# Performance work log

Hardware: AMD Instinct MI355X
Metric: run time of the kernel (lower is better)

## Reference

```python
import jax, jax.numpy as jnp
import numpy as np
from functools import partial

D_MODEL = 1024
D_HIDDEN = 4096
N_BLOCKS = 4
D_VOCAB = 32000
BATCH = 2
SEQ = 2048
LN_EPS = 1e-5
LRELU_SLOPE = 0.01  # torch nn.LeakyReLU default


def setup_inputs() -> dict:
    key = jax.random.key(0)
    ks = jax.random.split(key, 16)
    d, h, L, v = D_MODEL, D_HIDDEN, N_BLOCKS, D_VOCAB
    scale = d ** 0.5
    inp = {
        "tokens": jax.random.randint(ks[0], (BATCH, SEQ), 0, v, dtype=jnp.int64)
                  if jax.config.jax_enable_x64 else
                  jax.random.randint(ks[0], (BATCH, SEQ), 0, v, dtype=jnp.int32),
        "emb": jax.random.normal(ks[1], (v, d), jnp.float32) * 0.02,
        # per-block stacked params (leading axis = layer) for lax.scan
        "qk": jax.random.normal(ks[2], (L, d, d), jnp.float32) / scale,
        "ov": jax.random.normal(ks[3], (L, d, d), jnp.float32) / scale,
        "w_up": jax.random.normal(ks[4], (L, d, h), jnp.float32) / scale,
        "b_up": jnp.zeros((L, h), jnp.float32),
        "w_hid": jax.random.normal(ks[5], (L, h, h), jnp.float32) / (h ** 0.5),
        "b_hid": jnp.zeros((L, h), jnp.float32),
        "w_down": jax.random.normal(ks[6], (L, h, d), jnp.float32) / (h ** 0.5),
        "b_down": jnp.zeros((L, d), jnp.float32),
        "ln1_g": jnp.ones((L, d), jnp.float32),
        "ln1_b": jnp.zeros((L, d), jnp.float32),
        "ln2_g": jnp.ones((L, d), jnp.float32),
        "ln2_b": jnp.zeros((L, d), jnp.float32),
    }
    return inp


def _layer_norm(x, g, b):
    mu = jnp.mean(x, axis=-1, keepdims=True)
    var = jnp.mean(jnp.square(x - mu), axis=-1, keepdims=True)
    return (x - mu) * jax.lax.rsqrt(var + LN_EPS) * g + b


def _forward(tokens, emb, qk, ov, w_up, b_up, w_hid, b_hid, w_down, b_down,
             ln1_g, ln1_b, ln2_g, ln2_b):
    x = emb[tokens]                                   # [B, S, D]
    seq = tokens.shape[1]
    scale = jnp.asarray(D_MODEL ** 0.5, x.dtype)
    causal = jnp.tril(jnp.ones((seq, seq), bool))     # True = keep

    def block(x, p):
        (qk, ov, w_up, b_up, w_hid, b_hid, w_down, b_down,
         g1, b1, g2, b2) = p
        h = _layer_norm(x, g1, b1)
        # attention: (h @ qk @ h^T) / sqrt(d), causal mask, softmax, @ h @ ov
        scores = jnp.einsum('bsd,de,bte->bst', h, qk, h) / scale
        scores = jnp.where(causal, scores, -jnp.inf)
        attn = jax.nn.softmax(scores, axis=-1)
        x = x + jnp.einsum('bst,btd,de->bse', attn, h, ov)
        # MLP with LeakyReLU after every layer (incl. output)
        m = _layer_norm(x, g2, b2)
        m = jax.nn.leaky_relu(m @ w_up + b_up, LRELU_SLOPE)
        m = jax.nn.leaky_relu(m @ w_hid + b_hid, LRELU_SLOPE)
        m = jax.nn.leaky_relu(m @ w_down + b_down, LRELU_SLOPE)
        return x + m, None

    params = (qk, ov, w_up, b_up, w_hid, b_hid, w_down, b_down,
              ln1_g, ln1_b, ln2_g, ln2_b)
    x, _ = jax.lax.scan(block, x, params)
    return x @ emb.T                                  # [B, S, V] logits


@jax.jit
def reference(tokens, emb, qk, ov, w_up, b_up, w_hid, b_hid, w_down, b_down,
              ln1_g, ln1_b, ln2_g, ln2_b):
    return _forward(tokens, emb, qk, ov, w_up, b_up, w_hid, b_hid,
                    w_down, b_down, ln1_g, ln1_b, ln2_g, ln2_b)
```

## Files before the change

### kernel.cpp

```cpp
#include <hip/hip_runtime.h>

#define BS   4096
#define SEQL 2048
#define DM   1024
#define DH   4096
#define NV   32000

using u16 = unsigned short;

typedef __attribute__((ext_vector_type(8))) short bf16x8;
typedef __attribute__((ext_vector_type(4))) float f32x4;

__device__ __forceinline__ u16 f2b(float f) {
  union { float f; unsigned u; } c; c.f = f;
  unsigned u = c.u;
  u = (u + 0x7FFFu + ((u >> 16) & 1u)) >> 16;
  return (u16)u;
}

__device__ __forceinline__ void gld16(const u16* g, u16* l) {
  __builtin_amdgcn_global_load_lds(
      (__attribute__((address_space(1))) void*)(void*)const_cast<u16*>(g),
      (__attribute__((address_space(3))) void*)l, 16, 0, 0);
}

__global__ __launch_bounds__(256) void k_embed(const int* __restrict__ tok,
                                               const float* __restrict__ emb,
                                               float* __restrict__ x) {
  const long row = blockIdx.x;
  const long e = tok[row];
  ((float4*)(x + row * DM))[threadIdx.x] = ((const float4*)(emb + e * DM))[threadIdx.x];
}

__global__ __launch_bounds__(256) void k_cvt(const float* __restrict__ in,
                                             u16* __restrict__ out, int n4) {
  int i = blockIdx.x * 256 + threadIdx.x;
  if (i < n4) {
    float4 v = ((const float4*)in)[i];
    ushort4 o;
    o.x = f2b(v.x); o.y = f2b(v.y); o.z = f2b(v.z); o.w = f2b(v.w);
    ((ushort4*)out)[i] = o;
  }
}

__global__ __launch_bounds__(256) void k_ln(const float* __restrict__ x,
                                            const float* __restrict__ g,
                                            const float* __restrict__ b,
                                            u16* __restrict__ out) {
  const long row = blockIdx.x;
  const int t = threadIdx.x;
  float4 v = ((const float4*)(x + row * DM))[t];
  float s  = v.x + v.y + v.z + v.w;
  float q2 = v.x*v.x + v.y*v.y + v.z*v.z + v.w*v.w;
#pragma unroll
  for (int o = 1; o < 64; o <<= 1) { s += __shfl_xor(s, o); q2 += __shfl_xor(q2, o); }
  __shared__ float rs_[4], rq_[4];
  const int lane = t & 63, wid = t >> 6;
  if (lane == 0) { rs_[wid] = s; rq_[wid] = q2; }
  __syncthreads();
  s  = rs_[0] + rs_[1] + rs_[2] + rs_[3];
  q2 = rq_[0] + rq_[1] + rq_[2] + rq_[3];
  const float mu   = s * (1.f / 1024.f);
  const float var  = q2 * (1.f / 1024.f) - mu * mu;
  const float rstd = rsqrtf(var + 1e-5f);
  float4 gg = ((const float4*)g)[t];
  float4 bb = ((const float4*)b)[t];
  ushort4 o;
  o.x = f2b((v.x - mu) * rstd * gg.x + bb.x);
  o.y = f2b((v.y - mu) * rstd * gg.y + bb.y);
  o.z = f2b((v.z - mu) * rstd * gg.z + bb.z);
  o.w = f2b((v.w - mu) * rstd * gg.w + bb.w);
  ((ushort4*)(out + row * DM))[t] = o;
}

__device__ __forceinline__ u16 to_b16(float v) { return f2b(v); }
__device__ __forceinline__ u16 to_b16(u16 v)   { return v; }

template <typename T>
__global__ __launch_bounds__(256) void k_transpose(const T* __restrict__ in,
                                                   u16* __restrict__ out,
                                                   int R, int C, long inz, long outz) {
  __shared__ u16 tile[32][33];
  const T* ip = in + (long)blockIdx.z * inz;
  u16* op = out + (long)blockIdx.z * outz;
  const int tx = threadIdx.x & 31, ty = threadIdx.x >> 5;
  const long c0 = (long)blockIdx.x * 32, r0 = (long)blockIdx.y * 32;
#pragma unroll
  for (int i = 0; i < 4; ++i)
    tile[ty + i * 8][tx] = to_b16(ip[(r0 + ty + i * 8) * C + c0 + tx]);
  __syncthreads();
#pragma unroll
  for (int i = 0; i < 4; ++i)
    op[(c0 + ty + i * 8) * R + r0 + tx] = tile[tx][ty + i * 8];
}

__global__ __launch_bounds__(256) void k_softmax(const float* __restrict__ sc,
                                                 u16* __restrict__ at) {
  const int r = blockIdx.x;
  const long z = blockIdx.y;
  const int t = threadIdx.x;
  const float* row = sc + (z * SEQL + r) * SEQL;
  u16* orow = at + (z * SEQL + r) * SEQL;
  float vals[8];
  float mx = -3.4e38f;
#pragma unroll
  for (int i = 0; i < 8; ++i) {
    int c = i * 256 + t;
    float v = (c <= r) ? row[c] : -3.4e38f;
    vals[i] = v;
    mx = fmaxf(mx, v);
  }
#pragma unroll
  for (int o = 1; o < 64; o <<= 1) mx = fmaxf(mx, __shfl_xor(mx, o));
  __shared__ float rm[4], rsum[4];
  const int lane = t & 63, wid = t >> 6;
  if (lane == 0) rm[wid] = mx;
  __syncthreads();
  mx = fmaxf(fmaxf(rm[0], rm[1]), fmaxf(rm[2], rm[3]));
  float sum = 0.f;
#pragma unroll
  for (int i = 0; i < 8; ++i) {
    int c = i * 256 + t;
    float e = (c <= r) ? __expf(vals[i] - mx) : 0.f;
    vals[i] = e;
    sum += e;
  }
#pragma unroll
  for (int o = 1; o < 64; o <<= 1) sum += __shfl_xor(sum, o);
  if (lane == 0) rsum[wid] = sum;
  __syncthreads();
  sum = rsum[0] + rsum[1] + rsum[2] + rsum[3];
  const float inv = 1.f / sum;
#pragma unroll
  for (int i = 0; i < 8; ++i) orow[i * 256 + t] = f2b(vals[i] * inv);
}

template <int EPI, bool BIAS, bool LRELU, int CAUSAL>
__global__ __launch_bounds__(256, 2) void k_gemm_bt(
    const u16* __restrict__ A, const u16* __restrict__ B, void* __restrict__ C,
    const float* __restrict__ bias, int K, int N,
    long sAz, long sBz, long sCz, float scale) {
  __shared__ u16 lA[128 * 32];
  __shared__ u16 lB[128 * 32];
  const int t = threadIdx.x;
  const long z = blockIdx.z;
  const long row0 = (long)blockIdx.x * 128;
  const long col0 = (long)blockIdx.y * 128;
  if (CAUSAL == 1 && col0 > row0 + 127) return;
  const int Klim = (CAUSAL == 2) ? min(K, (int)row0 + 128) : K;
  const u16* Ab = A + z * sAz;
  const u16* Bb = B + z * sBz;

  const int rr = t >> 2;
  const int c8 = (t & 3) * 8;
  const u16* gA0 = Ab + (row0 + rr) * K + c8;
  const u16* gA1 = Ab + (row0 + 64 + rr) * K + c8;
  const u16* gB0 = Bb + (col0 + rr) * K + c8;
  const u16* gB1 = Bb + (col0 + 64 + rr) * K + c8;
  u16* sA0 = &lA[rr * 32 + c8];
  u16* sA1 = &lA[(64 + rr) * 32 + c8];
  u16* sB0 = &lB[rr * 32 + c8];
  u16* sB1 = &lB[(64 + rr) * 32 + c8];

  const int lane = t & 63;
  const int w = t >> 6;
  const int wr = (w >> 1) * 64, wc = (w & 1) * 64;
  const int fr = lane & 15;
  const int fk = (lane >> 4) * 8;

  f32x4 acc[4][4] = {};

  for (int k0 = 0; k0 < Klim; k0 += 32) {
    gld16(gA0 + k0, sA0);
    gld16(gA1 + k0, sA1);
    gld16(gB0 + k0, sB0);
    gld16(gB1 + k0, sB1);
    __syncthreads();
    bf16x8 av[4], bv[4];
#pragma unroll
    for (int m = 0; m < 4; ++m) av[m] = *(const bf16x8*)&lA[(wr + m * 16 + fr) * 32 + fk];
#pragma unroll
    for (int n = 0; n < 4; ++n) bv[n] = *(const bf16x8*)&lB[(wc + n * 16 + fr) * 32 + fk];
#pragma unroll
    for (int m = 0; m < 4; ++m)
#pragma unroll
      for (int n = 0; n < 4; ++n)
        acc[m][n] = __builtin_amdgcn_mfma_f32_16x16x32_bf16(av[m], bv[n], acc[m][n], 0, 0, 0);
    __syncthreads();
  }

  const int er = (lane >> 4) * 4;
  const int ec = lane & 15;
#pragma unroll
  for (int m = 0; m < 4; ++m) {
#pragma unroll
    for (int n = 0; n < 4; ++n) {
#pragma unroll
      for (int j = 0; j < 4; ++j) {
        long r = row0 + wr + m * 16 + er + j;
        long c = col0 + wc + n * 16 + ec;
        float v = acc[m][n][j] * scale;
        if (BIAS)  v += bias[c];
        if (LRELU) v = v > 0.f ? v : 0.01f * v;
        if (EPI == 0)      ((float*)C)[z * sCz + r * (long)N + c] = v;
        else if (EPI == 1) ((u16*)C)[z * sCz + r * (long)N + c] = f2b(v);
        else               ((float*)C)[z * sCz + r * (long)N + c] += v;
      }
    }
  }
}

template <int EPI, bool BIAS, bool LRELU>
__global__ __launch_bounds__(512, 2) void k_gemm256(
    const u16* __restrict__ A, const u16* __restrict__ B, void* __restrict__ C,
    const float* __restrict__ bias, int K, int N, float scale) {
  __shared__ u16 S[2][2][16384];
  const int t = threadIdx.x;
  const int lane = t & 63;
  const int w = t >> 6;
  const int wr = w >> 2;
  const int wc = w & 3;
  const long row0 = (long)blockIdx.x * 256;
  const long col0 = (long)blockIdx.y * 256;
  const int nt = K >> 6;

  const u16* pA[4];
  const u16* pB[4];
  int ldsoff[4];
#pragma unroll
  for (int i = 0; i < 4; ++i) {
    int d = t * 16 + i * 8192;
    int dx = d ^ (((d >> 7) & 7) << 4);
    int srow = dx >> 7;
    int scol = (dx & 127) >> 1;
    ldsoff[i] = d >> 1;
    pA[i] = A + (row0 + srow) * (long)K + scol;
    pB[i] = B + (col0 + srow) * (long)K + scol;
  }

  const int fr = lane & 15;
  const int fky = lane >> 4;
  const int axor = (fr & 7) << 4;
  const int abase = (wr * 128 + fr) * 128 + fky * 16;
  const int bbase = (wc * 64 + fr) * 128 + fky * 16;

  f32x4 acc[8][4] = {};

  auto STAGE = [&](int b) {
    u16* SA = &S[b][0][0];
    u16* SB = &S[b][1][0];
#pragma unroll
    for (int i = 0; i < 4; ++i) gld16(pA[i], SA + ldsoff[i]);
#pragma unroll
    for (int i = 0; i < 4; ++i) gld16(pB[i], SB + ldsoff[i]);
#pragma unroll
    for (int i = 0; i < 4; ++i) { pA[i] += 64; pB[i] += 64; }
  };

  auto COMPUTE = [&](int b) {
    const char* Ab = (const char*)&S[b][0][0];
    const char* Bb = (const char*)&S[b][1][0];
    bf16x8 bv[8];
#pragma unroll
    for (int n = 0; n < 4; ++n)
#pragma unroll
      for (int kk = 0; kk < 2; ++kk)
        bv[n * 2 + kk] = *(const bf16x8*)(Bb + ((bbase + n * 2048 + kk * 64) ^ axor));
    __builtin_amdgcn_s_setprio(1);
#pragma unroll
    for (int m = 0; m < 8; ++m) {
      bf16x8 a0 = *(const bf16x8*)(Ab + ((abase + m * 2048) ^ axor));
      bf16x8 a1 = *(const bf16x8*)(Ab + ((abase + m * 2048 + 64) ^ axor));
#pragma unroll
      for (int n = 0; n < 4; ++n)
        acc[m][n] = __builtin_amdgcn_mfma_f32_16x16x32_bf16(a0, bv[n * 2], acc[m][n], 0, 0, 0);
#pragma unroll
      for (int n = 0; n < 4; ++n)
        acc[m][n] = __builtin_amdgcn_mfma_f32_16x16x32_bf16(a1, bv[n * 2 + 1], acc[m][n], 0, 0, 0);
    }
    __builtin_amdgcn_s_setprio(0);
  };

  STAGE(0);
  __syncthreads();
  int cur = 0;
  for (int tt = 0; tt < nt; ++tt) {
    if (tt + 1 < nt) STAGE(cur ^ 1);
    COMPUTE(cur);
    __syncthreads();
    cur ^= 1;
  }

  const int er = (lane >> 4) * 4;
  const int ec = lane & 15;
#pragma unroll
  for (int m = 0; m < 8; ++m) {
#pragma unroll
    for (int n = 0; n < 4; ++n) {
#pragma unroll
      for (int j = 0; j < 4; ++j) {
        long r = row0 + wr * 128 + m * 16 + er + j;
        long c = col0 + wc * 64 + n * 16 + ec;
        float v = acc[m][n][j] * scale;
        if (BIAS)  v += bias[c];
        if (LRELU) v = v > 0.f ? v : 0.01f * v;
        if (EPI == 0)      ((float*)C)[r * (long)N + c] = v;
        else if (EPI == 1) ((u16*)C)[r * (long)N + c] = f2b(v);
        else               ((float*)C)[r * (long)N + c] += v;
      }
    }
  }
}

extern "C" void kernel_launch(void* const* d_in, const int* in_sizes, int n_in,
                              void* d_out, int out_size, void* d_ws, size_t ws_size,
                              hipStream_t stream) {
  const int*   tokens = (const int*)d_in[0];
  const float* emb    = (const float*)d_in[1];
  const float* qk     = (const float*)d_in[2];
  const float* ov     = (const float*)d_in[3];
  const float* wup    = (const float*)d_in[4];
  const float* bup    = (const float*)d_in[5];
  const float* whid   = (const float*)d_in[6];
  const float* bhid   = (const float*)d_in[7];
  const float* wdown  = (const float*)d_in[8];
  const float* bdown  = (const float*)d_in[9];
  const float* g1     = (const float*)d_in[10];
  const float* b1     = (const float*)d_in[11];
  const float* g2     = (const float*)d_in[12];
  const float* b2     = (const float*)d_in[13];

  char* Ob = (char*)d_out;
  float* scores = (float*)(Ob + 0);
  u16*   attn   = (u16*)(Ob + 33554432);
  u16*   m1     = (u16*)(Ob + 50331648);
  u16*   m2     = (u16*)(Ob + 83886080);
  u16*   qkT    = (u16*)(Ob + 117440512);
  u16*   ovT    = (u16*)(Ob + 125829120);
  u16*   upT    = (u16*)(Ob + 134217728);
  u16*   hidT   = (u16*)(Ob + 167772160);
  u16*   downT  = (u16*)(Ob + 301989888);
  float* xres   = (float*)(Ob + 335544320);
  u16*   h      = (u16*)(Ob + 352321536);
  u16*   hT     = (u16*)(Ob + 360710144);
  u16*   q      = (u16*)(Ob + 369098752);
  u16*   attnV  = (u16*)(Ob + 377487360);

  u16* embB = (u16*)d_ws;
  u16* xB   = (u16*)((char*)d_ws + 65536000);

  k_embed<<<dim3(BS), 256, 0, stream>>>(tokens, emb, xres);
  k_cvt<<<dim3(32000), 256, 0, stream>>>(emb, embB, 8192000);

  k_transpose<float><<<dim3(32, 32, 4),   256, 0, stream>>>(qk,    qkT,   1024, 1024, 1048576,  1048576);
  k_transpose<float><<<dim3(32, 32, 4),   256, 0, stream>>>(ov,    ovT,   1024, 1024, 1048576,  1048576);
  k_transpose<float><<<dim3(128, 32, 4),  256, 0, stream>>>(wup,   upT,   1024, 4096, 4194304,  4194304);
  k_transpose<float><<<dim3(128, 128, 4), 256, 0, stream>>>(whid,  hidT,  4096, 4096, 16777216, 16777216);
  k_transpose<float><<<dim3(32, 128, 4),  256, 0, stream>>>(wdown, downT, 4096, 1024, 4194304,  4194304);

  for (int l = 0; l < 4; ++l) {
    k_ln<<<dim3(BS), 256, 0, stream>>>(xres, g1 + l * 1024, b1 + l * 1024, h);
    k_transpose<u16><<<dim3(32, 64, 2), 256, 0, stream>>>(h, hT, 2048, 1024, 2048L * 1024, 1024L * 2048);
    k_gemm_bt<1, false, false, 0><<<dim3(32, 8, 1), 256, 0, stream>>>(
        h, qkT + (long)l * 1048576, q, nullptr, 1024, 1024, 0, 0, 0, 0.03125f);
    k_gemm_bt<0, false, false, 1><<<dim3(16, 16, 2), 256, 0, stream>>>(
        q, h, scores, nullptr, 1024, 2048, 2048L * 1024, 2048L * 1024, 2048L * 2048, 1.f);
    k_softmax<<<dim3(2048, 2), 256, 0, stream>>>(scores, attn);
    k_gemm_bt<1, false, false, 2><<<dim3(16, 8, 2), 256, 0, stream>>>(
        attn, hT, attnV, nullptr, 2048, 1024, 2048L * 2048, 1024L * 2048, 2048L * 1024, 1.f);
    k_gemm_bt<2, false, false, 0><<<dim3(32, 8, 1), 256, 0, stream>>>(
        attnV, ovT + (long)l * 1048576, xres, nullptr, 1024, 1024, 0, 0, 0, 1.f);

    k_ln<<<dim3(BS), 256, 0, stream>>>(xres, g2 + l * 1024, b2 + l * 1024, h);
    k_gemm256<1, true, true><<<dim3(16, 16), 512, 0, stream>>>(
        h, upT + (long)l * 4194304, m1, bup + l * 4096, 1024, 4096, 1.f);
    k_gemm256<1, true, true><<<dim3(16, 16), 512, 0, stream>>>(
        m1, hidT + (long)l * 16777216, m2, bhid + l * 4096, 4096, 4096, 1.f);
    k_gemm_bt<2, true, true, 0><<<dim3(32, 8, 1), 256, 0, stream>>>(
        m2, downT + (long)l * 4194304, xres, bdown + l * 1024, 4096, 1024, 0, 0, 0, 1.f);
  }

  k_cvt<<<dim3(4096), 256, 0, stream>>>(xres, xB, 1048576);
  k_gemm256<0, false, false><<<dim3(16, 125), 512, 0, stream>>>(
      xB, embB, (float*)d_out, nullptr, 1024, 32000, 1.f);
}
```

Baseline: 2.120 ms.

## Restructure 256x256 GEMM into four-phase pipelined schedule with split-K LDS halves

Rewrites the main loop of the 256-tile GEMM so each K-step of 64 is split into two 32-wide halves and two M-halves, giving four phases. Each phase issues LDS reads, then one quarter of the next tile's global-to-LDS loads, then 16 MFMAs, with explicit s_barrier and vmcnt waits in place of __syncthreads. The LDS layout moves to 64-byte rows with a smaller XOR swizzle, offsets are precomputed, and launch bounds drop to one block per CU. The aim is finer interleaving of memory loads with MFMA work, at the cost of fewer resident waves and the risk of races if the vmcnt counting is wrong.

```diff
diff --git a/kernel.cpp b/kernel.cpp
--- a/kernel.cpp
+++ b/kernel.cpp
@@ -211,10 +211,11 @@
 }
 
 template <int EPI, bool BIAS, bool LRELU>
-__global__ __launch_bounds__(512, 2) void k_gemm256(
+__global__ __launch_bounds__(512, 1) void k_gemm256(
     const u16* __restrict__ A, const u16* __restrict__ B, void* __restrict__ C,
     const float* __restrict__ bias, int K, int N, float scale) {
-  __shared__ u16 S[2][2][16384];
+  __shared__ u16 S[65536];
+  char* Sc = (char*)&S[0];
   const int t = threadIdx.x;
   const int lane = t & 63;
   const int w = t >> 6;
@@ -224,72 +225,94 @@
   const long col0 = (long)blockIdx.y * 256;
   const int nt = K >> 6;
 
-  const u16* pA[4];
-  const u16* pB[4];
-  int ldsoff[4];
-#pragma unroll
-  for (int i = 0; i < 4; ++i) {
+  int srow[2], scol[2], ldsb[2];
+#pragma unroll
+  for (int i = 0; i < 2; ++i) {
     int d = t * 16 + i * 8192;
-    int dx = d ^ (((d >> 7) & 7) << 4);
-    int srow = dx >> 7;
-    int scol = (dx & 127) >> 1;
-    ldsoff[i] = d >> 1;
-    pA[i] = A + (row0 + srow) * (long)K + scol;
-    pB[i] = B + (col0 + srow) * (long)K + scol;
-  }
+    int dx = d ^ (((d >> 7) & 3) << 4);
+    srow[i] = dx >> 6;
+    scol[i] = (dx & 63) >> 1;
+    ldsb[i] = d;
+  }
+  const u16* Abase = A + row0 * (long)K;
+  const u16* Bbase = B + col0 * (long)K;
+
+  auto stage = [&](int opb, int kh, int buf, int kb) {
+#pragma unroll
+    for (int i = 0; i < 2; ++i) {
+      const u16* src = (opb ? Bbase : Abase) + (long)srow[i] * K + kb + kh * 32 + scol[i];
+      u16* dst = &S[(buf * 4 + opb * 2 + kh) * 8192 + (ldsb[i] >> 1)];
+      gld16(src, dst);
+    }
+  };
 
   const int fr = lane & 15;
   const int fky = lane >> 4;
-  const int axor = (fr & 7) << 4;
-  const int abase = (wr * 128 + fr) * 128 + fky * 16;
-  const int bbase = (wc * 64 + fr) * 128 + fky * 16;
+  const int axor = ((fr >> 1) & 3) << 4;
+  int aoff[8], boff[4];
+#pragma unroll
+  for (int m = 0; m < 8; ++m)
+    aoff[m] = (((wr * 128 + m * 16 + fr) * 64) + fky * 16) ^ axor;
+#pragma unroll
+  for (int n = 0; n < 4; ++n)
+    boff[n] = (((wc * 64 + n * 16 + fr) * 64) + fky * 16) ^ axor;
 
   f32x4 acc[8][4] = {};
 
-  auto STAGE = [&](int b) {
-    u16* SA = &S[b][0][0];
-    u16* SB = &S[b][1][0];
-#pragma unroll
-    for (int i = 0; i < 4; ++i) gld16(pA[i], SA + ldsoff[i]);
-#pragma unroll
-    for (int i = 0; i < 4; ++i) gld16(pB[i], SB + ldsoff[i]);
-#pragma unroll
-    for (int i = 0; i < 4; ++i) { pA[i] += 64; pB[i] += 64; }
-  };
-
-  auto COMPUTE = [&](int b) {
-    const char* Ab = (const char*)&S[b][0][0];
-    const char* Bb = (const char*)&S[b][1][0];
-    bf16x8 bv[8];
-#pragma unroll
-    for (int n = 0; n < 4; ++n)
-#pragma unroll
-      for (int kk = 0; kk < 2; ++kk)
-        bv[n * 2 + kk] = *(const bf16x8*)(Bb + ((bbase + n * 2048 + kk * 64) ^ axor));
-    __builtin_amdgcn_s_setprio(1);
-#pragma unroll
-    for (int m = 0; m < 8; ++m) {
-      bf16x8 a0 = *(const bf16x8*)(Ab + ((abase + m * 2048) ^ axor));
-      bf16x8 a1 = *(const bf16x8*)(Ab + ((abase + m * 2048 + 64) ^ axor));
-#pragma unroll
-      for (int n = 0; n < 4; ++n)
-        acc[m][n] = __builtin_amdgcn_mfma_f32_16x16x32_bf16(a0, bv[n * 2], acc[m][n], 0, 0, 0);
-#pragma unroll
-      for (int n = 0; n < 4; ++n)
-        acc[m][n] = __builtin_amdgcn_mfma_f32_16x16x32_bf16(a1, bv[n * 2 + 1], acc[m][n], 0, 0, 0);
-    }
-    __builtin_amdgcn_s_setprio(0);
-  };
-
-  STAGE(0);
-  __syncthreads();
-  int cur = 0;
+#define PHASE(kh, mh, sop, skh, guard, knext)                                    \
+  {                                                                              \
+    const char* Ah = Sc + cur * 65536 + (kh) * 16384;                            \
+    const char* Bh = Sc + cur * 65536 + 32768 + (kh) * 16384;                    \
+    bf16x8 av0 = *(const bf16x8*)(Ah + aoff[(mh) * 4 + 0]);                      \
+    bf16x8 av1 = *(const bf16x8*)(Ah + aoff[(mh) * 4 + 1]);                      \
+    bf16x8 av2 = *(const bf16x8*)(Ah + aoff[(mh) * 4 + 2]);                      \
+    bf16x8 av3 = *(const bf16x8*)(Ah + aoff[(mh) * 4 + 3]);                      \
+    bf16x8 bv0 = *(const bf16x8*)(Bh + boff[0]);                                 \
+    bf16x8 bv1 = *(const bf16x8*)(Bh + boff[1]);                                 \
+    bf16x8 bv2 = *(const bf16x8*)(Bh + boff[2]);                                 \
+    bf16x8 bv3 = *(const bf16x8*)(Bh + boff[3]);                                 \
+    stage(sop, skh, nxt, knext);                                                 \
+    __builtin_amdgcn_s_barrier();                                                \
+    __builtin_amdgcn_s_setprio(1);                                               \
+    acc[(mh)*4+0][0] = __builtin_amdgcn_mfma_f32_16x16x32_bf16(av0, bv0, acc[(mh)*4+0][0], 0, 0, 0); \
+    acc[(mh)*4+0][1] = __builtin_amdgcn_mfma_f32_16x16x32_bf16(av0, bv1, acc[(mh)*4+0][1], 0, 0, 0); \
+    acc[(mh)*4+0][2] = __builtin_amdgcn_mfma_f32_16x16x32_bf16(av0, bv2, acc[(mh)*4+0][2], 0, 0, 0); \
+    acc[(mh)*4+0][3] = __builtin_amdgcn_mfma_f32_16x16x32_bf16(av0, bv3, acc[(mh)*4+0][3], 0, 0, 0); \
+    acc[(mh)*4+1][0] = __builtin_amdgcn_mfma_f32_16x16x32_bf16(av1, bv0, acc[(mh)*4+1][0], 0, 0, 0); \
+    acc[(mh)*4+1][1] = __builtin_amdgcn_mfma_f32_16x16x32_bf16(av1, bv1, acc[(mh)*4+1][1], 0, 0, 0); \
+    acc[(mh)*4+1][2] = __builtin_amdgcn_mfma_f32_16x16x32_bf16(av1, bv2, acc[(mh)*4+1][2], 0, 0, 0); \
+    acc[(mh)*4+1][3] = __builtin_amdgcn_mfma_f32_16x16x32_bf16(av1, bv3, acc[(mh)*4+1][3], 0, 0, 0); \
+    acc[(mh)*4+2][0] = __builtin_amdgcn_mfma_f32_16x16x32_bf16(av2, bv0, acc[(mh)*4+2][0], 0, 0, 0); \
+    acc[(mh)*4+2][1] = __builtin_amdgcn_mfma_f32_16x16x32_bf16(av2, bv1, acc[(mh)*4+2][1], 0, 0, 0); \
+    acc[(mh)*4+2][2] = __builtin_amdgcn_mfma_f32_16x16x32_bf16(av2, bv2, acc[(mh)*4+2][2], 0, 0, 0); \
+    acc[(mh)*4+2][3] = __builtin_amdgcn_mfma_f32_16x16x32_bf16(av2, bv3, acc[(mh)*4+2][3], 0, 0, 0); \
+    acc[(mh)*4+3][0] = __builtin_amdgcn_mfma_f32_16x16x32_bf16(av3, bv0, acc[(mh)*4+3][0], 0, 0, 0); \
+    acc[(mh)*4+3][1] = __builtin_amdgcn_mfma_f32_16x16x32_bf16(av3, bv1, acc[(mh)*4+3][1], 0, 0, 0); \
+    acc[(mh)*4+3][2] = __builtin_amdgcn_mfma_f32_16x16x32_bf16(av3, bv2, acc[(mh)*4+3][2], 0, 0, 0); \
+    acc[(mh)*4+3][3] = __builtin_amdgcn_mfma_f32_16x16x32_bf16(av3, bv3, acc[(mh)*4+3][3], 0, 0, 0); \
+    __builtin_amdgcn_s_setprio(0);                                               \
+    if (guard) asm volatile("s_waitcnt vmcnt(4)" ::: "memory");                  \
+    __builtin_amdgcn_s_barrier();                                                \
+  }
+
+  stage(0, 0, 0, 0);
+  stage(1, 0, 0, 0);
+  stage(0, 1, 0, 0);
+  stage(1, 1, 0, 0);
+  asm volatile("s_waitcnt vmcnt(4)" ::: "memory");
+  __builtin_amdgcn_s_barrier();
+
+  int cur = 0, nxt = 1;
   for (int tt = 0; tt < nt; ++tt) {
-    if (tt + 1 < nt) STAGE(cur ^ 1);
-    COMPUTE(cur);
-    __syncthreads();
-    cur ^= 1;
-  }
+    const int knext = (tt + 1 < nt) ? (tt + 1) * 64 : tt * 64;
+    PHASE(0, 0, 0, 0, false, knext)
+    PHASE(0, 1, 1, 0, true,  knext)
+    PHASE(1, 0, 0, 1, false, knext)
+    PHASE(1, 1, 1, 1, true,  knext)
+    cur ^= 1; nxt ^= 1;
+  }
+  asm volatile("s_waitcnt vmcnt(0)" ::: "memory");
+#undef PHASE
 
   const int er = (lane >> 4) * 4;
   const int ec = lane & 15;
```

After: 2.171 ms. 1.02x slower.
